# Kernel optimization log

Measured on AMD Instinct MI355X. Metric: run time of the kernel, lower is better.

## Reference

```python
import jax, jax.numpy as jnp
import numpy as np

B, C, CW = 64, 862, 512
F_BINS = CW // 2 + 1          # 257 rfft bins -> embedding in_features
D_MODEL, N_HEADS, D_FF, N_LAYERS = 256, 16, 512, 3
EPS = 1e-5


def setup_inputs() -> dict:
    key = jax.random.key(0)
    ks = jax.random.split(key, 12)
    s = 0.02
    return {
        'x_re': jax.random.normal(ks[0], (B, C, F_BINS), jnp.float32),
        'x_im': jax.random.normal(ks[1], (B, C, F_BINS), jnp.float32),
        # complex embedding Linear(F_BINS, D_MODEL): weight [D_MODEL, F_BINS], bias [D_MODEL]
        'emb_Wre': jax.random.normal(ks[2], (D_MODEL, F_BINS), jnp.float32) * s,
        'emb_Wim': jax.random.normal(ks[3], (D_MODEL, F_BINS), jnp.float32) * s,
        'emb_bre': jax.random.normal(ks[4], (D_MODEL,), jnp.float32) * s,
        'emb_bim': jax.random.normal(ks[5], (D_MODEL,), jnp.float32) * s,
        # per-layer FFN weights (stacked over layers)
        'W1': jax.random.normal(ks[6], (N_LAYERS, D_FF, D_MODEL), jnp.float32) * s,
        'b1': jnp.zeros((N_LAYERS, D_FF), jnp.float32),
        'W2': jax.random.normal(ks[7], (N_LAYERS, D_MODEL, D_FF), jnp.float32) * s,
        'b2': jnp.zeros((N_LAYERS, D_MODEL), jnp.float32),
        # per-layer BatchNorm affine params (attn norm and ffn norm)
        'gamma1': jnp.ones((N_LAYERS, D_MODEL), jnp.float32),
        'beta1': jnp.zeros((N_LAYERS, D_MODEL), jnp.float32),
        'gamma2': jnp.ones((N_LAYERS, D_MODEL), jnp.float32),
        'beta2': jnp.zeros((N_LAYERS, D_MODEL), jnp.float32),
    }


def _batchnorm(x, g, b):
    # Transpose(1,2) + BatchNorm1d(d_model) + Transpose(1,2): normalize each
    # feature (last axis) over (batch, seq) with batch statistics (training mode).
    m = x.mean(axis=(0, 1))
    v = x.var(axis=(0, 1))  # biased, matching torch normalization
    return (x - m) * jax.lax.rsqrt(v + EPS) * g + b


def _encoder_layer(y, Wff1, bff1, Wff2, bff2, g1, be1, g2, be2):
    # y: [2b, c, d] -- real half stacked over imag half along dim 0
    scale = float(D_MODEL // N_HEADS) ** -0.5
    b = y.shape[0] // 2
    # _MultiheadAttention: q = src, k = flip(src, dims=[1,2]), v = src (no projections applied)
    k = jnp.flip(y, axis=(1, 2))
    q_re, q_im = y[:b], y[b:]
    k_re, k_im = k[:b], k[b:]
    v_re = y[:b]
    v_im = y[:b]  # faithful to source: both halves use v[:bs//2]
    asr = scale * (q_re * k_re - q_im * k_im)
    asi = scale * (q_re * k_im - q_im * k_re)  # minus, as written in source
    o_re = asr * v_re - asi * v_im
    o_im = asr * v_im + asi * v_re
    out = jnp.concatenate([o_re, o_im], axis=0)  # [2b, c, d]
    # transpose(1,2).contiguous().view(bs, -1, d_model): a data shuffle, kept faithfully
    out = jnp.swapaxes(out, 1, 2).reshape(out.shape[0], out.shape[1], out.shape[2])
    src = y + out                       # residual (dropout = 0)
    src = _batchnorm(src, g1, be1)      # post-norm (pre_norm=False)
    ff = jnp.einsum('bcd,fd->bcf', src, Wff1) + bff1
    ff = jax.nn.gelu(ff, approximate=False)
    ff = jnp.einsum('bcf,df->bcd', ff, Wff2) + bff2
    src = src + ff
    src = _batchnorm(src, g2, be2)
    return src


def reference(x_re, x_im, emb_Wre, emb_Wim, emb_bre, emb_bim,
              W1, b1, W2, b2, gamma1, beta1, gamma2, beta2):
    # complex Linear embedding: (x_re + i x_im) @ (Wre + i Wim)^T + (bre + i bim)
    y_re = x_re @ emb_Wre.T - x_im @ emb_Wim.T + emb_bre
    y_im = x_re @ emb_Wim.T + x_im @ emb_Wre.T + emb_bim
    y = jnp.concatenate([y_re, y_im], axis=0)  # [2b, c, d_model]
    for i in range(N_LAYERS):
        y = _encoder_layer(y, W1[i], b1[i], W2[i], b2[i],
                           gamma1[i], beta1[i], gamma2[i], beta2[i])
    b = x_re.shape[0]
    # torch.view_as_complex(stack([y[:b], y[b:]], -1)) -> return real/imag stacked
    return jnp.stack([y[:b], y[b:]], axis=-1)  # [b, c, d_model, 2]
```

## Files before the change

kernel.cpp:

```cpp
#include <hip/hip_runtime.h>
#include <hip/hip_bf16.h>
#include <math.h>

#define BB   64
#define CC   862
#define FB   257
#define DM   256
#define DFF  512
#define NIMG 128
#define ROWS_RE (BB*CC)
#define ROWS_ALL (NIMG*CC)
#define NELEM ((long)ROWS_ALL*DM)

typedef __bf16 bf16x8 __attribute__((ext_vector_type(8)));
typedef float  f32x4  __attribute__((ext_vector_type(4)));

__global__ __launch_bounds__(256) void k_wtrans(const float* __restrict__ Wre,
                                                const float* __restrict__ Wim,
                                                float2* __restrict__ Wt) {
  int f = blockIdx.x;
  int d = threadIdx.x;
  float2 w;
  w.x = Wre[(long)d * FB + f];
  w.y = Wim[(long)d * FB + f];
  Wt[(long)f * DM + d] = w;
}

__global__ __launch_bounds__(256) void k_wcvt(const float* __restrict__ W1,
                                              const float* __restrict__ W2,
                                              __bf16* __restrict__ W1b,
                                              __bf16* __restrict__ W2b) {
  long i = ((long)blockIdx.x * 256 + threadIdx.x) * 4;
  const long N1 = 3L * DFF * DM;
  const float* src;
  __bf16* dst;
  if (i < N1) { src = W1 + i; dst = W1b + i; }
  else        { src = W2 + (i - N1); dst = W2b + (i - N1); }
  float4 x = *(const float4*)src;
  dst[0] = (__bf16)x.x; dst[1] = (__bf16)x.y;
  dst[2] = (__bf16)x.z; dst[3] = (__bf16)x.w;
}

__global__ void k_ident(float* ss) {
  int d = threadIdx.x;
  ss[d] = 1.0f;
  ss[DM + d] = 0.0f;
}

__global__ __launch_bounds__(256) void k_emb(
    const float* __restrict__ xr, const float* __restrict__ xi,
    const float2* __restrict__ Wt,
    const float* __restrict__ bre, const float* __restrict__ bim,
    float* __restrict__ A) {
  __shared__ float sxr[16][260];
  __shared__ float sxi[16][260];
  int t = threadIdx.x;
  int lane = t & 63;
  int rg = t >> 6;
  int r0 = rg * 4;
  int d0 = lane * 4;
  long row0 = (long)blockIdx.x * 16;

  for (int idx = t; idx < 16 * FB; idx += 256) {
    int r = idx / FB, f = idx - r * FB;
    sxr[r][f] = xr[(row0 + r) * FB + f];
    sxi[r][f] = xi[(row0 + r) * FB + f];
  }
  __syncthreads();

  float ar[4][4], ai[4][4];
#pragma unroll
  for (int rr = 0; rr < 4; rr++)
#pragma unroll
    for (int j = 0; j < 4; j++) { ar[rr][j] = 0.f; ai[rr][j] = 0.f; }

  for (int f0 = 0; f0 < 256; f0 += 4) {
    float4 xr4[4], xi4[4];
#pragma unroll
    for (int rr = 0; rr < 4; rr++) {
      xr4[rr] = *(const float4*)&sxr[r0 + rr][f0];
      xi4[rr] = *(const float4*)&sxi[r0 + rr][f0];
    }
#pragma unroll
    for (int fl = 0; fl < 4; fl++) {
      const float4* wp = (const float4*)(Wt + (long)(f0 + fl) * DM + d0);
      float4 wA = wp[0];
      float4 wB = wp[1];
#pragma unroll
      for (int rr = 0; rr < 4; rr++) {
        float xrv = ((const float*)&xr4[rr])[fl];
        float xiv = ((const float*)&xi4[rr])[fl];
        ar[rr][0] = fmaf(xrv, wA.x, ar[rr][0]); ar[rr][0] = fmaf(-xiv, wA.y, ar[rr][0]);
        ai[rr][0] = fmaf(xrv, wA.y, ai[rr][0]); ai[rr][0] = fmaf( xiv, wA.x, ai[rr][0]);
        ar[rr][1] = fmaf(xrv, wA.z, ar[rr][1]); ar[rr][1] = fmaf(-xiv, wA.w, ar[rr][1]);
        ai[rr][1] = fmaf(xrv, wA.w, ai[rr][1]); ai[rr][1] = fmaf( xiv, wA.z, ai[rr][1]);
        ar[rr][2] = fmaf(xrv, wB.x, ar[rr][2]); ar[rr][2] = fmaf(-xiv, wB.y, ar[rr][2]);
        ai[rr][2] = fmaf(xrv, wB.y, ai[rr][2]); ai[rr][2] = fmaf( xiv, wB.x, ai[rr][2]);
        ar[rr][3] = fmaf(xrv, wB.z, ar[rr][3]); ar[rr][3] = fmaf(-xiv, wB.w, ar[rr][3]);
        ai[rr][3] = fmaf(xrv, wB.w, ai[rr][3]); ai[rr][3] = fmaf( xiv, wB.z, ai[rr][3]);
      }
    }
  }
  {
    const float4* wp = (const float4*)(Wt + (long)256 * DM + d0);
    float4 wA = wp[0];
    float4 wB = wp[1];
#pragma unroll
    for (int rr = 0; rr < 4; rr++) {
      float xrv = sxr[r0 + rr][256];
      float xiv = sxi[r0 + rr][256];
      ar[rr][0] = fmaf(xrv, wA.x, ar[rr][0]); ar[rr][0] = fmaf(-xiv, wA.y, ar[rr][0]);
      ai[rr][0] = fmaf(xrv, wA.y, ai[rr][0]); ai[rr][0] = fmaf( xiv, wA.x, ai[rr][0]);
      ar[rr][1] = fmaf(xrv, wA.z, ar[rr][1]); ar[rr][1] = fmaf(-xiv, wA.w, ar[rr][1]);
      ai[rr][1] = fmaf(xrv, wA.w, ai[rr][1]); ai[rr][1] = fmaf( xiv, wA.z, ai[rr][1]);
      ar[rr][2] = fmaf(xrv, wB.x, ar[rr][2]); ar[rr][2] = fmaf(-xiv, wB.y, ar[rr][2]);
      ai[rr][2] = fmaf(xrv, wB.y, ai[rr][2]); ai[rr][2] = fmaf( xiv, wB.x, ai[rr][2]);
      ar[rr][3] = fmaf(xrv, wB.z, ar[rr][3]); ar[rr][3] = fmaf(-xiv, wB.w, ar[rr][3]);
      ai[rr][3] = fmaf(xrv, wB.w, ai[rr][3]); ai[rr][3] = fmaf( xiv, wB.z, ai[rr][3]);
    }
  }

  float4 brv = ((const float4*)bre)[lane];
  float4 biv = ((const float4*)bim)[lane];
#pragma unroll
  for (int rr = 0; rr < 4; rr++) {
    long bc = row0 + r0 + rr;
    float4 o;
    o.x = ar[rr][0] + brv.x; o.y = ar[rr][1] + brv.y;
    o.z = ar[rr][2] + brv.z; o.w = ar[rr][3] + brv.w;
    *(float4*)(A + bc * DM + d0) = o;
    float4 oi;
    oi.x = ai[rr][0] + biv.x; oi.y = ai[rr][1] + biv.y;
    oi.z = ai[rr][2] + biv.z; oi.w = ai[rr][3] + biv.w;
    *(float4*)(A + (bc + (long)ROWS_RE) * DM + d0) = oi;
  }
}

__global__ __launch_bounds__(256) void k_attn(const float* __restrict__ A,
                                              const float* __restrict__ ss,
                                              float* __restrict__ T) {
  __shared__ float ore[32][33];
  __shared__ float oim[32][33];
  __shared__ float ssc[256];
  __shared__ float ssh[256];
  int tx = threadIdx.x;
  int ty = threadIdx.y;
  int t = ty * 32 + tx;
  ssc[t] = ss[t];
  ssh[t] = ss[DM + t];
  __syncthreads();

  int c0 = blockIdx.x * 32;
  int d0 = blockIdx.y * 32;
  int b  = blockIdx.z;
  const long base_re = (long)b * CC * DM;
  const long base_im = (long)(b + BB) * CC * DM;
  int d = d0 + tx;
  int kd = DM - 1 - d;
  float scq = ssc[d], shq = ssh[d];
  float sck = ssc[kd], shk = ssh[kd];
#pragma unroll
  for (int q = 0; q < 4; q++) {
    int cl = ty + 8 * q;
    int c = c0 + cl;
    if (c < CC) {
      float qr = fmaf(A[base_re + (long)c * DM + d], scq, shq);
      float qi = fmaf(A[base_im + (long)c * DM + d], scq, shq);
      float kr = fmaf(A[base_re + (long)(CC - 1 - c) * DM + kd], sck, shk);
      float ki = fmaf(A[base_im + (long)(CC - 1 - c) * DM + kd], sck, shk);
      float asr = 0.25f * (qr * kr - qi * ki);
      float asi = 0.25f * (qr * ki - qi * kr);
      ore[cl][tx] = (asr - asi) * qr;
      oim[cl][tx] = (asr + asi) * qr;
    }
  }
  __syncthreads();
#pragma unroll
  for (int q = 0; q < 4; q++) {
    int dl = ty + 8 * q;
    int dd = d0 + dl;
    int c = c0 + tx;
    if (c < CC) {
      long flat = (long)dd * CC + c;
      int dp = (int)(flat & 255);
      float sc = ssc[dp], sh = ssh[dp];
      T[base_re + flat] = fmaf(A[base_re + flat], sc, sh) + ore[tx][dl];
      T[base_im + flat] = fmaf(A[base_im + flat], sc, sh) + oim[tx][dl];
    }
  }
}

__global__ void k_zero(double* s) { s[threadIdx.x] = 0.0; }

__global__ __launch_bounds__(256) void k_bnstats(const float* __restrict__ P,
                                                 double* __restrict__ stats) {
  int d = threadIdx.x;
  long row0 = (long)blockIdx.x * 128;
  double s = 0.0, s2 = 0.0;
  for (int r = 0; r < 128; r++) {
    float x = P[(row0 + r) * DM + d];
    s += (double)x;
    s2 += (double)x * (double)x;
  }
  atomicAdd(&stats[d], s);
  atomicAdd(&stats[DM + d], s2);
}

__global__ void k_finalize(double* __restrict__ stats,
                           const float* __restrict__ g, const float* __restrict__ be,
                           float* __restrict__ ss) {
  int d = threadIdx.x;
  double n = (double)ROWS_ALL;
  double m = stats[d] / n;
  double v = stats[DM + d] / n - m * m;
  float inv = (float)(1.0 / sqrt(v + 1e-5));
  float sc = g[d] * inv;
  ss[d] = sc;
  ss[DM + d] = be[d] - (float)m * sc;
  stats[d] = 0.0;
  stats[DM + d] = 0.0;
}

__global__ __launch_bounds__(256) void k_bnfinal(const float* __restrict__ A,
                                                 const float* __restrict__ ss,
                                                 float* __restrict__ out) {
  long gid = (long)blockIdx.x * 256 + threadIdx.x;
  int d = (int)(gid & 255);
  long bc = gid >> 8;
  float sc = ss[d], sh = ss[DM + d];
  float re = A[bc * DM + d];
  float im = A[(bc + (long)ROWS_RE) * DM + d];
  float2 o;
  o.x = fmaf(re, sc, sh);
  o.y = fmaf(im, sc, sh);
  ((float2*)out)[gid] = o;
}

#define PS2 264
#define PH2 520

__global__ __launch_bounds__(512, 2) void k_ffm(
    const float* __restrict__ P, const float* __restrict__ ss,
    const __bf16* __restrict__ W1b, const float* __restrict__ b1,
    const __bf16* __restrict__ W2b, const float* __restrict__ b2,
    float* __restrict__ Out, double* __restrict__ stats) {
  __shared__ __bf16 sS[64 * PS2];
  __shared__ __bf16 sH[64 * PH2];
  int t = threadIdx.x;
  int lane = t & 63;
  int w = t >> 6;
  int half = lane >> 4;
  int l16 = lane & 15;
  long row0 = (long)blockIdx.x * 64;

  {
    const float4* Pv = (const float4*)(P + row0 * DM);
    const float4* scv = (const float4*)ss;
    const float4* shv = (const float4*)(ss + DM);
#pragma unroll
    for (int i = 0; i < 8; i++) {
      int v = t + i * 512;
      int r = v >> 6, k4 = v & 63;
      float4 x = Pv[(long)r * 64 + k4];
      float4 sc = scv[k4];
      float4 sh = shv[k4];
      x.x = fmaf(x.x, sc.x, sh.x);
      x.y = fmaf(x.y, sc.y, sh.y);
      x.z = fmaf(x.z, sc.z, sh.z);
      x.w = fmaf(x.w, sc.w, sh.w);
      __bf16* dst = &sS[r * PS2 + k4 * 4];
      dst[0] = (__bf16)x.x; dst[1] = (__bf16)x.y;
      dst[2] = (__bf16)x.z; dst[3] = (__bf16)x.w;
    }
  }
  __syncthreads();

  int n0 = w * 64;
  f32x4 acc[4][4];
#pragma unroll
  for (int mt = 0; mt < 4; mt++)
#pragma unroll
    for (int j = 0; j < 4; j++) acc[mt][j] = (f32x4){0.f, 0.f, 0.f, 0.f};

#pragma unroll 2
  for (int kt = 0; kt < 8; kt++) {
    int kb = kt * 32 + half * 8;
    bf16x8 a[4];
#pragma unroll
    for (int mt = 0; mt < 4; mt++)
      a[mt] = *(const bf16x8*)&sS[(mt * 16 + l16) * PS2 + kb];
#pragma unroll
    for (int j = 0; j < 4; j++) {
      bf16x8 bfr = *(const bf16x8*)&W1b[(long)(n0 + j * 16 + l16) * DM + kb];
#pragma unroll
      for (int mt = 0; mt < 4; mt++)
        acc[mt][j] = __builtin_amdgcn_mfma_f32_16x16x32_bf16(a[mt], bfr, acc[mt][j], 0, 0, 0);
    }
  }

  {
#pragma unroll
    for (int j = 0; j < 4; j++) {
      int f = n0 + j * 16 + l16;
      float b1v = b1[f];
#pragma unroll
      for (int mt = 0; mt < 4; mt++)
#pragma unroll
        for (int r = 0; r < 4; r++) {
          float x = acc[mt][j][r] + b1v;
          float u = x * (0.7978845608f + 0.0356774081f * x * x);
          float g = x / (1.0f + __expf(-2.0f * u));
          int m = mt * 16 + half * 4 + r;
          sH[m * PH2 + f] = (__bf16)g;
        }
    }
  }
  __syncthreads();

  int n2 = w * 32;
  f32x4 acc2[4][2];
#pragma unroll
  for (int mt = 0; mt < 4; mt++)
#pragma unroll
    for (int j = 0; j < 2; j++) acc2[mt][j] = (f32x4){0.f, 0.f, 0.f, 0.f};

#pragma unroll 2
  for (int kt = 0; kt < 16; kt++) {
    int kb = kt * 32 + half * 8;
    bf16x8 a[4];
#pragma unroll
    for (int mt = 0; mt < 4; mt++)
      a[mt] = *(const bf16x8*)&sH[(mt * 16 + l16) * PH2 + kb];
#pragma unroll
    for (int j = 0; j < 2; j++) {
      bf16x8 bfr = *(const bf16x8*)&W2b[(long)(n2 + j * 16 + l16) * DFF + kb];
#pragma unroll
      for (int mt = 0; mt < 4; mt++)
        acc2[mt][j] = __builtin_amdgcn_mfma_f32_16x16x32_bf16(a[mt], bfr, acc2[mt][j], 0, 0, 0);
    }
  }

  {
#pragma unroll
    for (int j = 0; j < 2; j++) {
      int d = n2 + j * 16 + l16;
      float b2v = b2[d];
      float sc = ss[d], sh = ss[DM + d];
      float s = 0.f, s2 = 0.f;
#pragma unroll
      for (int mt = 0; mt < 4; mt++)
#pragma unroll
        for (int r = 0; r < 4; r++) {
          int m = mt * 16 + half * 4 + r;
          long idx = (row0 + m) * DM + d;
          float vv = fmaf(P[idx], sc, sh) + acc2[mt][j][r] + b2v;
          Out[idx] = vv;
          s += vv;
          s2 += vv * vv;
        }
      s  += __shfl_xor(s, 16);  s  += __shfl_xor(s, 32);
      s2 += __shfl_xor(s2, 16); s2 += __shfl_xor(s2, 32);
      if (half == 0) {
        atomicAdd(&stats[d], (double)s);
        atomicAdd(&stats[DM + d], (double)s2);
      }
    }
  }
}

extern "C" void kernel_launch(void* const* d_in, const int* in_sizes, int n_in,
                              void* d_out, int out_size, void* d_ws, size_t ws_size,
                              hipStream_t stream) {
  const float* xr  = (const float*)d_in[0];
  const float* xi  = (const float*)d_in[1];
  const float* Wre = (const float*)d_in[2];
  const float* Wim = (const float*)d_in[3];
  const float* bre = (const float*)d_in[4];
  const float* bim = (const float*)d_in[5];
  const float* W1  = (const float*)d_in[6];
  const float* b1  = (const float*)d_in[7];
  const float* W2  = (const float*)d_in[8];
  const float* b2  = (const float*)d_in[9];
  const float* g1  = (const float*)d_in[10];
  const float* be1 = (const float*)d_in[11];
  const float* g2  = (const float*)d_in[12];
  const float* be2 = (const float*)d_in[13];

  float* A = (float*)d_ws;
  double* stats = (double*)((char*)d_ws + (size_t)NELEM * 4);
  float* ss = (float*)(stats + 512);
  __bf16* W1b = (__bf16*)(ss + 512);
  __bf16* W2b = W1b + 3L * DFF * DM;
  float* T = (float*)d_out;
  float2* Wt = (float2*)d_out;

  k_wtrans<<<FB, 256, 0, stream>>>(Wre, Wim, Wt);
  k_emb<<<ROWS_RE / 16, 256, 0, stream>>>(xr, xi, Wt, bre, bim, A);
  k_zero<<<1, 512, 0, stream>>>(stats);
  k_ident<<<1, 256, 0, stream>>>(ss);
  k_wcvt<<<768, 256, 0, stream>>>(W1, W2, W1b, W2b);

  for (int l = 0; l < 3; l++) {
    k_attn<<<dim3(27, 8, 64), dim3(32, 8), 0, stream>>>(A, ss, T);
    k_bnstats<<<862, 256, 0, stream>>>(T, stats);
    k_finalize<<<1, 256, 0, stream>>>(stats, g1 + l * DM, be1 + l * DM, ss);
    k_ffm<<<ROWS_ALL / 64, 512, 0, stream>>>(T, ss,
                                             W1b + (long)l * DFF * DM, b1 + l * DFF,
                                             W2b + (long)l * DFF * DM, b2 + l * DM,
                                             A, stats);
    k_finalize<<<1, 256, 0, stream>>>(stats, g2 + l * DM, be2 + l * DM, ss);
    if (l == 2) {
      k_bnfinal<<<ROWS_RE * DM / 256, 256, 0, stream>>>(A, ss, (float*)d_out);
    }
  }
}
```

Measured before the change: 1.484 ms.

## Rewrite complex embedding as bf16 MFMA GEMM with stacked real/imag weights

Recasts the complex embedding as one real GEMM with K=514 (padded to 544): the activation row is [x_re | x_im] and the weight matrix stacks [Wre, -Wim; Wim, Wre] into 512 output columns, converted to bf16. The embedding then runs on MFMA 16x16x32 bf16 instructions with 64-row tiles staged in LDS, replacing the scalar fp32 FMA loop. This removes a compute-bound CUDA-core GEMM, at the cost of bf16 rounding of the inputs and embedding weights and of scattered scalar fp32 output stores.

Measured after the change: 1.244 ms. -16.1%, faster.

```diff
diff --git a/kernel.cpp b/kernel.cpp
--- a/kernel.cpp
+++ b/kernel.cpp
@@ -14,17 +14,6 @@
 
 typedef __bf16 bf16x8 __attribute__((ext_vector_type(8)));
 typedef float  f32x4  __attribute__((ext_vector_type(4)));
-
-__global__ __launch_bounds__(256) void k_wtrans(const float* __restrict__ Wre,
-                                                const float* __restrict__ Wim,
-                                                float2* __restrict__ Wt) {
-  int f = blockIdx.x;
-  int d = threadIdx.x;
-  float2 w;
-  w.x = Wre[(long)d * FB + f];
-  w.y = Wim[(long)d * FB + f];
-  Wt[(long)f * DM + d] = w;
-}
 
 __global__ __launch_bounds__(256) void k_wcvt(const float* __restrict__ W1,
                                               const float* __restrict__ W2,
@@ -47,92 +36,88 @@
   ss[DM + d] = 0.0f;
 }
 
-__global__ __launch_bounds__(256) void k_emb(
+#define KE 544
+#define PE 552
+
+__global__ __launch_bounds__(256) void k_wemb(const float* __restrict__ Wre,
+                                              const float* __restrict__ Wim,
+                                              __bf16* __restrict__ Wb) {
+  int n = blockIdx.x;
+  int d = n & 255;
+  bool im = (n >= 256);
+  const float* Wa = im ? Wim : Wre;
+  const float* Wc = im ? Wre : Wim;
+  float sgn = im ? 1.0f : -1.0f;
+  for (int k = threadIdx.x; k < KE; k += 256) {
+    float v;
+    if (k < 257)      v = Wa[(long)d * FB + k];
+    else if (k < 514) v = sgn * Wc[(long)d * FB + (k - 257)];
+    else              v = 0.0f;
+    Wb[(long)n * KE + k] = (__bf16)v;
+  }
+}
+
+__global__ __launch_bounds__(512, 2) void k_embm(
     const float* __restrict__ xr, const float* __restrict__ xi,
-    const float2* __restrict__ Wt,
+    const __bf16* __restrict__ Wb,
     const float* __restrict__ bre, const float* __restrict__ bim,
     float* __restrict__ A) {
-  __shared__ float sxr[16][260];
-  __shared__ float sxi[16][260];
+  __shared__ __bf16 sA[64 * PE];
   int t = threadIdx.x;
   int lane = t & 63;
-  int rg = t >> 6;
-  int r0 = rg * 4;
-  int d0 = lane * 4;
-  long row0 = (long)blockIdx.x * 16;
-
-  for (int idx = t; idx < 16 * FB; idx += 256) {
-    int r = idx / FB, f = idx - r * FB;
-    sxr[r][f] = xr[(row0 + r) * FB + f];
-    sxi[r][f] = xi[(row0 + r) * FB + f];
+  int w = t >> 6;
+  int half = lane >> 4;
+  int l16 = lane & 15;
+  long row0 = (long)blockIdx.x * 64;
+
+  for (int idx = t; idx < 64 * 30; idx += 512) {
+    int r = idx / 30, j = idx - r * 30;
+    sA[r * PE + 514 + j] = (__bf16)0.f;
+  }
+  for (int idx = t; idx < 64 * 257; idx += 512) {
+    int r = idx / 257, f = idx - r * 257;
+    long g = (row0 + r) * FB + f;
+    sA[r * PE + f]       = (__bf16)xr[g];
+    sA[r * PE + 257 + f] = (__bf16)xi[g];
   }
   __syncthreads();
 
-  float ar[4][4], ai[4][4];
-#pragma unroll
-  for (int rr = 0; rr < 4; rr++)
-#pragma unroll
-    for (int j = 0; j < 4; j++) { ar[rr][j] = 0.f; ai[rr][j] = 0.f; }
-
-  for (int f0 = 0; f0 < 256; f0 += 4) {
-    float4 xr4[4], xi4[4];
-#pragma unroll
-    for (int rr = 0; rr < 4; rr++) {
-      xr4[rr] = *(const float4*)&sxr[r0 + rr][f0];
-      xi4[rr] = *(const float4*)&sxi[r0 + rr][f0];
-    }
-#pragma unroll
-    for (int fl = 0; fl < 4; fl++) {
-      const float4* wp = (const float4*)(Wt + (long)(f0 + fl) * DM + d0);
-      float4 wA = wp[0];
-      float4 wB = wp[1];
-#pragma unroll
-      for (int rr = 0; rr < 4; rr++) {
-        float xrv = ((const float*)&xr4[rr])[fl];
-        float xiv = ((const float*)&xi4[rr])[fl];
-        ar[rr][0] = fmaf(xrv, wA.x, ar[rr][0]); ar[rr][0] = fmaf(-xiv, wA.y, ar[rr][0]);
-        ai[rr][0] = fmaf(xrv, wA.y, ai[rr][0]); ai[rr][0] = fmaf( xiv, wA.x, ai[rr][0]);
-        ar[rr][1] = fmaf(xrv, wA.z, ar[rr][1]); ar[rr][1] = fmaf(-xiv, wA.w, ar[rr][1]);
-        ai[rr][1] = fmaf(xrv, wA.w, ai[rr][1]); ai[rr][1] = fmaf( xiv, wA.z, ai[rr][1]);
-        ar[rr][2] = fmaf(xrv, wB.x, ar[rr][2]); ar[rr][2] = fmaf(-xiv, wB.y, ar[rr][2]);
-        ai[rr][2] = fmaf(xrv, wB.y, ai[rr][2]); ai[rr][2] = fmaf( xiv, wB.x, ai[rr][2]);
-        ar[rr][3] = fmaf(xrv, wB.z, ar[rr][3]); ar[rr][3] = fmaf(-xiv, wB.w, ar[rr][3]);
-        ai[rr][3] = fmaf(xrv, wB.w, ai[rr][3]); ai[rr][3] = fmaf( xiv, wB.z, ai[rr][3]);
+  int n0 = w * 64;
+  f32x4 acc[4][4];
+#pragma unroll
+  for (int mt = 0; mt < 4; mt++)
+#pragma unroll
+    for (int j = 0; j < 4; j++) acc[mt][j] = (f32x4){0.f, 0.f, 0.f, 0.f};
+
+#pragma unroll 1
+  for (int kt = 0; kt < 17; kt++) {
+    int kb = kt * 32 + half * 8;
+    bf16x8 a[4];
+#pragma unroll
+    for (int mt = 0; mt < 4; mt++)
+      a[mt] = *(const bf16x8*)&sA[(mt * 16 + l16) * PE + kb];
+#pragma unroll
+    for (int j = 0; j < 4; j++) {
+      bf16x8 bfr = *(const bf16x8*)&Wb[(long)(n0 + j * 16 + l16) * KE + kb];
+#pragma unroll
+      for (int mt = 0; mt < 4; mt++)
+        acc[mt][j] = __builtin_amdgcn_mfma_f32_16x16x32_bf16(a[mt], bfr, acc[mt][j], 0, 0, 0);
+    }
+  }
+
+#pragma unroll
+  for (int j = 0; j < 4; j++) {
+    int n = n0 + j * 16 + l16;
+    int d = n & 255;
+    float bv = (n < 256) ? bre[d] : bim[d];
+    long rbase = (n < 256) ? 0L : (long)ROWS_RE;
+#pragma unroll
+    for (int mt = 0; mt < 4; mt++)
+#pragma unroll
+      for (int r = 0; r < 4; r++) {
+        int m = mt * 16 + half * 4 + r;
+        A[(row0 + m + rbase) * DM + d] = acc[mt][j][r] + bv;
       }
-    }
-  }
-  {
-    const float4* wp = (const float4*)(Wt + (long)256 * DM + d0);
-    float4 wA = wp[0];
-    float4 wB = wp[1];
-#pragma unroll
-    for (int rr = 0; rr < 4; rr++) {
-      float xrv = sxr[r0 + rr][256];
-      float xiv = sxi[r0 + rr][256];
-      ar[rr][0] = fmaf(xrv, wA.x, ar[rr][0]); ar[rr][0] = fmaf(-xiv, wA.y, ar[rr][0]);
-      ai[rr][0] = fmaf(xrv, wA.y, ai[rr][0]); ai[rr][0] = fmaf( xiv, wA.x, ai[rr][0]);
-      ar[rr][1] = fmaf(xrv, wA.z, ar[rr][1]); ar[rr][1] = fmaf(-xiv, wA.w, ar[rr][1]);
-      ai[rr][1] = fmaf(xrv, wA.w, ai[rr][1]); ai[rr][1] = fmaf( xiv, wA.z, ai[rr][1]);
-      ar[rr][2] = fmaf(xrv, wB.x, ar[rr][2]); ar[rr][2] = fmaf(-xiv, wB.y, ar[rr][2]);
-      ai[rr][2] = fmaf(xrv, wB.y, ai[rr][2]); ai[rr][2] = fmaf( xiv, wB.x, ai[rr][2]);
-      ar[rr][3] = fmaf(xrv, wB.z, ar[rr][3]); ar[rr][3] = fmaf(-xiv, wB.w, ar[rr][3]);
-      ai[rr][3] = fmaf(xrv, wB.w, ai[rr][3]); ai[rr][3] = fmaf( xiv, wB.z, ai[rr][3]);
-    }
-  }
-
-  float4 brv = ((const float4*)bre)[lane];
-  float4 biv = ((const float4*)bim)[lane];
-#pragma unroll
-  for (int rr = 0; rr < 4; rr++) {
-    long bc = row0 + r0 + rr;
-    float4 o;
-    o.x = ar[rr][0] + brv.x; o.y = ar[rr][1] + brv.y;
-    o.z = ar[rr][2] + brv.z; o.w = ar[rr][3] + brv.w;
-    *(float4*)(A + bc * DM + d0) = o;
-    float4 oi;
-    oi.x = ai[rr][0] + biv.x; oi.y = ai[rr][1] + biv.y;
-    oi.z = ai[rr][2] + biv.z; oi.w = ai[rr][3] + biv.w;
-    *(float4*)(A + (bc + (long)ROWS_RE) * DM + d0) = oi;
   }
 }
 
@@ -392,13 +377,13 @@
   __bf16* W1b = (__bf16*)(ss + 512);
   __bf16* W2b = W1b + 3L * DFF * DM;
   float* T = (float*)d_out;
-  float2* Wt = (float2*)d_out;
-
-  k_wtrans<<<FB, 256, 0, stream>>>(Wre, Wim, Wt);
-  k_emb<<<ROWS_RE / 16, 256, 0, stream>>>(xr, xi, Wt, bre, bim, A);
+  __bf16* Wb = (__bf16*)d_out;
+
+  k_wemb<<<512, 256, 0, stream>>>(Wre, Wim, Wb);
+  k_wcvt<<<768, 256, 0, stream>>>(W1, W2, W1b, W2b);
   k_zero<<<1, 512, 0, stream>>>(stats);
   k_ident<<<1, 256, 0, stream>>>(ss);
-  k_wcvt<<<768, 256, 0, stream>>>(W1, W2, W1b, W2b);
+  k_embm<<<ROWS_RE / 64, 512, 0, stream>>>(xr, xi, Wb, bre, bim, A);
 
   for (int l = 0; l < 3; l++) {
     k_attn<<<dim3(27, 8, 64), dim3(32, 8), 0, stream>>>(A, ss, T);
```
